# Kernel optimization log

Hardware: AMD Instinct MI355X
Metric: run time of the kernel (lower is better)

Reference implementation:

```python
import jax, jax.numpy as jnp
import numpy as np

GRANULARITY = 50
PERCENTILES = (0.01, 0.99)


def setup_inputs() -> dict:
    key = jax.random.key(0)
    H = W = 6144
    sp = jax.random.uniform(key, (H, W), dtype=jnp.float32)
    return {
        "signal_probabilities": sp,
        "rho_max": jnp.float32(H - 1),
        "rho_min": jnp.float32(0.0),
        "theta_min_horizontal": jnp.float32(0.01),
        "theta_max_horizontal": jnp.float32(0.05),
        "theta_min_vertical": jnp.float32(1.52),
        "theta_max_vertical": jnp.float32(1.56),
    }


def _linspace(a, b, n):
    t = jnp.arange(n, dtype=jnp.float32) / (n - 1)
    return a + (b - a) * t


def _fix_edge_effects(buf):
    buf = buf.at[0, :].set(buf[1, :])
    buf = buf.at[-1, :].set(buf[-2, :])
    buf = buf.at[:, 0].set(buf[:, 1])
    buf = buf.at[:, -1].set(buf[:, -2])
    return buf


def _fill_buffer(H, W, thetas, rhos, mode):
    # vectorized over all granularity lines at once (no python loop over lines)
    if mode == "horizontal":
        y = jnp.arange(H)
        # x[g, H]: x = -y*tan(theta) + rho/cos(theta)
        x = -y[None, :] * jnp.tan(thetas)[:, None] + (rhos / jnp.cos(thetas))[:, None]
        x = jnp.clip(jnp.round(x).astype(jnp.int32), 0, W - 1)
        yb = jnp.broadcast_to(y[None, :], x.shape)
        buf = jnp.zeros((H, W), jnp.int32).at[yb, x].add(1)
        buf = jnp.cumsum(buf, axis=1)
    else:
        x = jnp.arange(W)
        # y[g, W]: y = -x/tan(theta) + rho/sin(theta)
        y = -x[None, :] / jnp.tan(thetas)[:, None] + (rhos / jnp.sin(thetas))[:, None]
        y = jnp.clip(jnp.round(y).astype(jnp.int32), 0, H - 1)
        xb = jnp.broadcast_to(x[None, :], y.shape)
        buf = jnp.zeros((H, W), jnp.int32).at[y, xb].add(1)
        buf = jnp.cumsum(buf, axis=0)
    return _fix_edge_effects(buf)


def _get_bounds(nsp, thetas, rhos, mode):
    g = GRANULARITY
    H, W = nsp.shape
    buf = _fill_buffer(H, W, thetas, rhos, mode)
    # segment-sum replaces the dense one_hot * probs reduction (same math)
    values = jax.ops.segment_sum(nsp.reshape(-1), buf.reshape(-1), num_segments=g)
    c = jnp.cumsum(values) / jnp.sum(values)
    lower = jnp.argmax(c >= PERCENTILES[0])  # first index with cumsum >= p0
    upper = (g - 1) - jnp.argmax((c <= PERCENTILES[1])[::-1]) + 2  # last index with cumsum <= p1, +2
    return lower, upper


def _take_neg(a, i):
    # a[-i] with python-style negative indexing (i == 0 -> a[0])
    g = a.shape[0]
    return jnp.take(a, (g - i) % g)


def _intersect(r1, t1, r2, t2):
    det = jnp.cos(t1) * jnp.sin(t2) - jnp.cos(t2) * jnp.sin(t1)
    x = (r1 * jnp.sin(t2) - r2 * jnp.sin(t1)) / det
    y = (r2 * jnp.cos(t1) - r1 * jnp.cos(t2)) / det
    return jnp.stack((x, y))


def reference(signal_probabilities, rho_max, rho_min, theta_min_horizontal,
              theta_max_horizontal, theta_min_vertical, theta_max_vertical):
    g = GRANULARITY
    nsp = signal_probabilities - signal_probabilities.min()
    nsp = nsp / nsp.sum()
    rhos = _linspace(rho_max, rho_min, g)
    th = _linspace(theta_min_horizontal, theta_max_horizontal, g)
    tv = _linspace(theta_min_vertical, theta_max_vertical, g)
    lh, uh = _get_bounds(nsp, th, rhos, "horizontal")
    lv, uv = _get_bounds(nsp, tv, rhos, "vertical")
    r_min_h, r_max_h = _take_neg(rhos, lh), _take_neg(rhos, uh)
    t_min_h, t_max_h = _take_neg(th, lh), _take_neg(th, uh)
    r_min_v, r_max_v = _take_neg(rhos, lv), _take_neg(rhos, uv)
    t_min_v, t_max_v = _take_neg(tv, lv), _take_neg(tv, uv)
    # [top-left, top-right, bottom-right, bottom-left] -> shape (4, 2)
    return jnp.stack([
        _intersect(r_min_h, t_min_h, r_min_v, t_min_v),
        _intersect(r_max_h, t_max_h, r_min_v, t_min_v),
        _intersect(r_max_h, t_max_h, r_max_v, t_max_v),
        _intersect(r_min_h, t_min_h, r_max_v, t_max_v),
    ], axis=0)
```

## Files before the change

### kernel.cpp

```cpp
#include <hip/hip_runtime.h>
#include <math.h>

#define HH 6144
#define WW 6144
constexpr int G = 50;
constexpr int NCOPY = 64;
constexpr int NG = NCOPY * G;
constexpr int BIG = 0x0FFFFFFF;
constexpr int MINBASE = 4 * NG;
constexpr int CTR = MINBASE + NCOPY;
constexpr int MASTER = CTR + NCOPY;
constexpr int C0 = MASTER + 2;

constexpr int TPB  = 384;
constexpr int PXT  = 16;
constexpr int NBLK = HH;

__device__ inline void ldsAddF(float* p, float v)      { __hip_atomic_fetch_add(p, v, __ATOMIC_RELAXED, __HIP_MEMORY_SCOPE_WORKGROUP); }
__device__ inline void ldsAddU(unsigned* p, unsigned v){ __hip_atomic_fetch_add(p, v, __ATOMIC_RELAXED, __HIP_MEMORY_SCOPE_WORKGROUP); }
__device__ inline void ldsMinU(unsigned* p, unsigned v){ __hip_atomic_fetch_min(p, v, __ATOMIC_RELAXED, __HIP_MEMORY_SCOPE_WORKGROUP); }
__device__ inline void glbAddF(float* p, float v)      { __hip_atomic_fetch_add(p, v, __ATOMIC_RELAXED, __HIP_MEMORY_SCOPE_AGENT); }
__device__ inline void glbAddU(unsigned* p, unsigned v){ __hip_atomic_fetch_add(p, v, __ATOMIC_RELAXED, __HIP_MEMORY_SCOPE_AGENT); }
__device__ inline void glbMinU(unsigned* p, unsigned v){ __hip_atomic_fetch_min(p, v, __ATOMIC_RELAXED, __HIP_MEMORY_SCOPE_AGENT); }
__device__ inline unsigned glbAddCtr(unsigned* p)      { return __hip_atomic_fetch_add(p, 1u, __ATOMIC_RELAXED, __HIP_MEMORY_SCOPE_AGENT); }
__device__ inline float atomLoadF(const float* p)      { return __hip_atomic_load(p, __ATOMIC_RELAXED, __HIP_MEMORY_SCOPE_AGENT); }
__device__ inline unsigned atomLoadU(const unsigned* p){ return __hip_atomic_load(p, __ATOMIC_RELAXED, __HIP_MEMORY_SCOPE_AGENT); }

__global__ void crop_init(unsigned int* __restrict__ ws,
                          const float* __restrict__ p_rmax,
                          const float* __restrict__ p_rmin,
                          const float* __restrict__ p_thmin,
                          const float* __restrict__ p_thmax,
                          const float* __restrict__ p_tvmin,
                          const float* __restrict__ p_tvmax) {
  int i = blockIdx.x * 256 + threadIdx.x;
  if (i < MINBASE) ws[i] = 0u;
  else if (i < MINBASE + NCOPY) ws[i] = 0x7F800000u;
  else if (i < C0) ws[i] = 0u;

  if (blockIdx.x == 0 && threadIdx.x < G) {
    int t = threadIdx.x;
    double u    = (double)t / (double)(G - 1);
    double rmax = (double)p_rmax[0], rmin = (double)p_rmin[0];
    double rho  = rmax + (rmin - rmax) * u;
    double th   = (double)p_thmin[0] + ((double)p_thmax[0] - (double)p_thmin[0]) * u;
    double tv   = (double)p_tvmin[0] + ((double)p_tvmax[0] - (double)p_tvmin[0]) * u;
    double cth = cos(th), sth = sin(th);
    double ctv = cos(tv), stv = sin(tv);
    double* dT   = (double*)(ws + C0);
    double* dRC  = (double*)(ws + C0 + 100);
    float*  fva  = (float*)(ws + C0 + 200);
    float*  fvb  = (float*)(ws + C0 + 250);
    double* dRho = (double*)(ws + C0 + 300);
    double* dSth = (double*)(ws + C0 + 400);
    double* dCth = (double*)(ws + C0 + 500);
    double* dStv = (double*)(ws + C0 + 600);
    double* dCtv = (double*)(ws + C0 + 700);
    dT[t]  = tan(th);
    dRC[t] = rho / cth;
    fva[t] = (float)(rho / stv);
    fvb[t] = (float)(ctv / stv);
    dRho[t] = rho; dSth[t] = sth; dCth[t] = cth; dStv[t] = stv; dCtv[t] = ctv;
  }
}

__launch_bounds__(TPB)
__global__ void crop_main(const float* __restrict__ sp,
                          float* __restrict__ wsf,
                          float* __restrict__ out) {
  __shared__ int pxh[G], pxv[G];
  __shared__ float hsum[G + 1], vsum[G + 1];
  __shared__ unsigned int hcnt[G + 1], vcnt[G + 1];
  __shared__ unsigned int blockMinBits;
  __shared__ double valD[100];

  const int t  = threadIdx.x;
  const int y  = blockIdx.x;
  const int yp = min(max(y, 1), HH - 2);
  const float fyp = (float)yp;
  const int x0 = t * PXT;

  const float4* p4 = (const float4*)(sp + (size_t)y * WW + x0);
  float4 q0 = p4[0], q1 = p4[1], q2 = p4[2], q3 = p4[3];

  for (int i = t; i < G + 1; i += TPB) { hsum[i] = 0.f; vsum[i] = 0.f; hcnt[i] = 0u; vcnt[i] = 0u; }
  if (t == TPB - 1) blockMinBits = 0x7F800000u;

  const unsigned int* wsu = (const unsigned int*)wsf;
  if (t < G) {
    const double* dT  = (const double*)(wsu + C0);
    const double* dRC = (const double*)(wsu + C0 + 100);
    const float*  fva = (const float*)(wsu + C0 + 200);
    const float*  fvb = (const float*)(wsu + C0 + 250);

    double xg = rint(fma(-(double)yp, dT[t], dRC[t]));
    xg = fmin(fmax(xg, 0.0), (double)(WW - 1));
    int xi = (int)xg;
    pxh[t] = (xi <= 1) ? 0 : (xi >= WW - 1 ? BIG : xi);

    float va = fva[t], vb = fvb[t];
    int lo = 1, hi = WW - 1;
    while (lo < hi) {
      int m = (lo + hi) >> 1;
      float yv = rintf(fmaf(-(float)m, vb, va));
      yv = fminf(fmaxf(yv, 0.f), (float)(HH - 1));
      if (yv <= fyp) hi = m; else lo = m + 1;
    }
    pxv[t] = (lo >= WW - 1) ? BIG : (lo == 1 ? 0 : lo);
  }
  __syncthreads();

  float px[PXT] = { q0.x,q0.y,q0.z,q0.w, q1.x,q1.y,q1.z,q1.w,
                    q2.x,q2.y,q2.z,q2.w, q3.x,q3.y,q3.z,q3.w };

  int lo = 0, hi = G;
  while (lo < hi) { int m = (lo + hi) >> 1; if (pxh[m] <= x0) hi = m; else lo = m + 1; }
  const int lbh = lo;
  const int nbh = (lbh > 0) ? pxh[lbh - 1] : BIG;
  const int kh  = min(nbh - x0, PXT);

  lo = 0; hi = G;
  while (lo < hi) { int m = (lo + hi) >> 1; if (pxv[m] <= x0) hi = m; else lo = m + 1; }
  const int lbv = lo;
  const int nbv = (lbv > 0) ? pxv[lbv - 1] : BIG;
  const int kv  = min(nbv - x0, PXT);

  const int sh = G - lbh, sv = G - lbv;

  float S = 0.f, Ah = 0.f, Av = 0.f, mn = 3.4e38f;
#pragma unroll
  for (int k = 0; k < PXT; ++k) {
    float v = px[k];
    mn = fminf(mn, v);
    S += v;
    if (k + 1 == kh) Ah = S;
    if (k + 1 == kv) Av = S;
  }

  ldsAddF(&hsum[sh], Ah); ldsAddU(&hcnt[sh], (unsigned)kh);
  if (kh < PXT) { ldsAddF(&hsum[sh + 1], S - Ah); ldsAddU(&hcnt[sh + 1], (unsigned)(PXT - kh)); }
  ldsAddF(&vsum[sv], Av); ldsAddU(&vcnt[sv], (unsigned)kv);
  if (kv < PXT) { ldsAddF(&vsum[sv + 1], S - Av); ldsAddU(&vcnt[sv + 1], (unsigned)(PXT - kv)); }

  for (int off = 32; off; off >>= 1) mn = fminf(mn, __shfl_down(mn, off));
  if ((t & 63) == 0) ldsMinU(&blockMinBits, __float_as_uint(mn));

  __syncthreads();

  if (t >= 64) return;

  const int copy = y & (NCOPY - 1);
  unsigned int* wsw = (unsigned int*)wsf;
  if (t < G) {
    glbAddF(&wsf[copy * G + t], hsum[t]);
    glbAddU(&wsw[2 * NG + copy * G + t], hcnt[t]);
    glbAddF(&wsf[NG + copy * G + t], vsum[t]);
    glbAddU(&wsw[3 * NG + copy * G + t], vcnt[t]);
  }
  if (t == 0) glbMinU(&wsw[MINBASE + copy], blockMinBits);

  asm volatile("s_waitcnt vmcnt(0)" ::: "memory");

  int last = 0;
  if (t == 0) {
    unsigned p1 = glbAddCtr(&wsw[CTR + copy]);
    if (p1 == (unsigned)(NBLK / NCOPY - 1)) {
      unsigned p2 = glbAddCtr(&wsw[MASTER]);
      last = (p2 == (unsigned)(NCOPY - 1));
    }
  }
  last = __shfl(last, 0);
  if (!last) return;

  float vmn = __uint_as_float(atomLoadU(&wsu[MINBASE + t]));
  for (int off = 32; off; off >>= 1) vmn = fminf(vmn, __shfl_down(vmn, off));
  const double mv = (double)__shfl(vmn, 0);

  for (int p = t; p < 100; p += 64) {
    const int fam = p >= G;
    const int g = fam ? p - G : p;
    const int sumBase = fam ? NG : 0;
    const int cntBase = (2 + fam) * NG;
    double s = 0.0; unsigned c = 0;
#pragma unroll 8
    for (int cp = 0; cp < NCOPY; ++cp) {
      s += (double)atomLoadF(&wsf[sumBase + cp * G + g]);
      c += atomLoadU(&wsu[cntBase + cp * G + g]);
    }
    valD[p] = s - mv * (double)c;
  }
  asm volatile("s_waitcnt lgkmcnt(0)" ::: "memory");
  __builtin_amdgcn_sched_barrier(0);

  if (t == 0) {
    auto bounds = [&](int base, int& lowerI, int& upperI) {
      double tot = 0;
      for (int s = 0; s < G; ++s) tot += valD[base + s];
      double c = 0; bool found = false; int lastI = -1; lowerI = 0;
      for (int s = 0; s < G; ++s) {
        c += valD[base + s];
        double cc = c / tot;
        if (!found && cc >= 0.01) { lowerI = s; found = true; }
        if (cc <= 0.99) lastI = s;
      }
      upperI = (lastI < 0) ? (G + 1) : (lastI + 2);
    };
    int lh, uh, lv, uv;
    bounds(0, lh, uh);
    bounds(G, lv, uv);

    const double* dRho = (const double*)(wsu + C0 + 300);
    const double* dSth = (const double*)(wsu + C0 + 400);
    const double* dCth = (const double*)(wsu + C0 + 500);
    const double* dStv = (const double*)(wsu + C0 + 600);
    const double* dCtv = (const double*)(wsu + C0 + 700);

    auto tn = [&](int i) { return ((G - i) % G + G) % G; };
    int ihmin = tn(lh), ihmax = tn(uh), ivmin = tn(lv), ivmax = tn(uv);

    auto inter = [&](int ih, int iv, float* o) {
      double r1 = dRho[ih], s1 = dSth[ih], c1 = dCth[ih];
      double r2 = dRho[iv], s2 = dStv[iv], c2 = dCtv[iv];
      double det = c1 * s2 - c2 * s1;
      o[0] = (float)((r1 * s2 - r2 * s1) / det);
      o[1] = (float)((r2 * c1 - r1 * c2) / det);
    };
    inter(ihmin, ivmin, out + 0);
    inter(ihmax, ivmin, out + 2);
    inter(ihmax, ivmax, out + 4);
    inter(ihmin, ivmax, out + 6);
  }
}

extern "C" void kernel_launch(void* const* d_in, const int* in_sizes, int n_in,
                              void* d_out, int out_size, void* d_ws, size_t ws_size,
                              hipStream_t stream) {
  const float* sp    = (const float*)d_in[0];
  const float* rmax  = (const float*)d_in[1];
  const float* rmin  = (const float*)d_in[2];
  const float* thmin = (const float*)d_in[3];
  const float* thmax = (const float*)d_in[4];
  const float* tvmin = (const float*)d_in[5];
  const float* tvmax = (const float*)d_in[6];
  float* wsf  = (float*)d_ws;
  float* outp = (float*)d_out;

  crop_init<<<(C0 + 255) / 256, 256, 0, stream>>>((unsigned int*)d_ws,
                                                  rmax, rmin, thmin, thmax, tvmin, tvmax);
  crop_main<<<NBLK, TPB, 0, stream>>>(sp, wsf, outp);
}
```

Measured before the change: 251.6 us.

## Precompute per-row line boundaries in separate kernel and drop block barriers

```diff
diff --git a/kernel.cpp b/kernel.cpp
--- a/kernel.cpp
+++ b/kernel.cpp
@@ -11,14 +11,16 @@
 constexpr int CTR = MINBASE + NCOPY;
 constexpr int MASTER = CTR + NCOPY;
 constexpr int C0 = MASTER + 2;
+constexpr int PXHB = C0 + 800;
+constexpr int PXVB = PXHB + HH * G;
 
 constexpr int TPB  = 384;
 constexpr int PXT  = 16;
 constexpr int NBLK = HH;
+constexpr unsigned WPC = (HH / NCOPY) * (TPB / 64);
 
 __device__ inline void ldsAddF(float* p, float v)      { __hip_atomic_fetch_add(p, v, __ATOMIC_RELAXED, __HIP_MEMORY_SCOPE_WORKGROUP); }
 __device__ inline void ldsAddU(unsigned* p, unsigned v){ __hip_atomic_fetch_add(p, v, __ATOMIC_RELAXED, __HIP_MEMORY_SCOPE_WORKGROUP); }
-__device__ inline void ldsMinU(unsigned* p, unsigned v){ __hip_atomic_fetch_min(p, v, __ATOMIC_RELAXED, __HIP_MEMORY_SCOPE_WORKGROUP); }
 __device__ inline void glbAddF(float* p, float v)      { __hip_atomic_fetch_add(p, v, __ATOMIC_RELAXED, __HIP_MEMORY_SCOPE_AGENT); }
 __device__ inline void glbAddU(unsigned* p, unsigned v){ __hip_atomic_fetch_add(p, v, __ATOMIC_RELAXED, __HIP_MEMORY_SCOPE_AGENT); }
 __device__ inline void glbMinU(unsigned* p, unsigned v){ __hip_atomic_fetch_min(p, v, __ATOMIC_RELAXED, __HIP_MEMORY_SCOPE_AGENT); }
@@ -64,69 +66,84 @@
   }
 }
 
+__global__ void crop_bounds(unsigned int* __restrict__ ws) {
+  const int idx = blockIdx.x * 256 + threadIdx.x;
+  if (idx >= HH * G) return;
+  const int row = idx / G, g = idx - row * G;
+  const int yq = min(max(row, 1), HH - 2);
+  const float fyq = (float)yq;
+
+  const double* dT  = (const double*)(ws + C0);
+  const double* dRC = (const double*)(ws + C0 + 100);
+  const float*  fva = (const float*)(ws + C0 + 200);
+  const float*  fvb = (const float*)(ws + C0 + 250);
+
+  double xg = rint(fma(-(double)yq, dT[g], dRC[g]));
+  xg = fmin(fmax(xg, 0.0), (double)(WW - 1));
+  int xi = (int)xg;
+  ((int*)ws)[PXHB + idx] = (xi <= 1) ? 0 : (xi >= WW - 1 ? BIG : xi);
+
+  float va = fva[g], vb = fvb[g];
+  int lo = 1, hi = WW - 1;
+  while (lo < hi) {
+    int m = (lo + hi) >> 1;
+    float yv = rintf(fmaf(-(float)m, vb, va));
+    yv = fminf(fmaxf(yv, 0.f), (float)(HH - 1));
+    if (yv <= fyq) hi = m; else lo = m + 1;
+  }
+  ((int*)ws)[PXVB + idx] = (lo >= WW - 1) ? BIG : (lo == 1 ? 0 : lo);
+}
+
 __launch_bounds__(TPB)
 __global__ void crop_main(const float* __restrict__ sp,
                           float* __restrict__ wsf,
                           float* __restrict__ out) {
-  __shared__ int pxh[G], pxv[G];
-  __shared__ float hsum[G + 1], vsum[G + 1];
-  __shared__ unsigned int hcnt[G + 1], vcnt[G + 1];
-  __shared__ unsigned int blockMinBits;
+  __shared__ float    sH[TPB / 64][G + 2], sV[TPB / 64][G + 2];
+  __shared__ unsigned cH[TPB / 64][G + 2], cV[TPB / 64][G + 2];
   __shared__ double valD[100];
 
-  const int t  = threadIdx.x;
-  const int y  = blockIdx.x;
-  const int yp = min(max(y, 1), HH - 2);
-  const float fyp = (float)yp;
+  const int t = threadIdx.x, y = blockIdx.x;
+  const int w = t >> 6, lane = t & 63;
   const int x0 = t * PXT;
 
   const float4* p4 = (const float4*)(sp + (size_t)y * WW + x0);
   float4 q0 = p4[0], q1 = p4[1], q2 = p4[2], q3 = p4[3];
 
-  for (int i = t; i < G + 1; i += TPB) { hsum[i] = 0.f; vsum[i] = 0.f; hcnt[i] = 0u; vcnt[i] = 0u; }
-  if (t == TPB - 1) blockMinBits = 0x7F800000u;
-
-  const unsigned int* wsu = (const unsigned int*)wsf;
-  if (t < G) {
-    const double* dT  = (const double*)(wsu + C0);
-    const double* dRC = (const double*)(wsu + C0 + 100);
-    const float*  fva = (const float*)(wsu + C0 + 200);
-    const float*  fvb = (const float*)(wsu + C0 + 250);
-
-    double xg = rint(fma(-(double)yp, dT[t], dRC[t]));
-    xg = fmin(fmax(xg, 0.0), (double)(WW - 1));
-    int xi = (int)xg;
-    pxh[t] = (xi <= 1) ? 0 : (xi >= WW - 1 ? BIG : xi);
-
-    float va = fva[t], vb = fvb[t];
-    int lo = 1, hi = WW - 1;
-    while (lo < hi) {
-      int m = (lo + hi) >> 1;
-      float yv = rintf(fmaf(-(float)m, vb, va));
-      yv = fminf(fmaxf(yv, 0.f), (float)(HH - 1));
-      if (yv <= fyp) hi = m; else lo = m + 1;
-    }
-    pxv[t] = (lo >= WW - 1) ? BIG : (lo == 1 ? 0 : lo);
-  }
-  __syncthreads();
+  const int* ph = (const int*)wsf + PXHB + y * G;
+  const int* pv = (const int*)wsf + PXVB + y * G;
+  int bh = (lane < G) ? ph[lane] : BIG;
+  int bv = (lane < G) ? pv[lane] : BIG;
+
+  if (lane < G + 2) { sH[w][lane] = 0.f; cH[w][lane] = 0u; sV[w][lane] = 0.f; cV[w][lane] = 0u; }
+
+  int lo = 0, hi = G;
+#pragma unroll
+  for (int it = 0; it < 6; ++it) {
+    int m = (lo + hi) >> 1;
+    int pm = __shfl(bh, m);
+    if (lo < hi) { if (pm <= x0) hi = m; else lo = m + 1; }
+  }
+  const int lbh = lo;
+  int nbp = __shfl(bh, lbh > 0 ? lbh - 1 : 0);
+  const int nbh = (lbh > 0) ? nbp : BIG;
+  const int kh  = min(nbh - x0, PXT);
+
+  lo = 0; hi = G;
+#pragma unroll
+  for (int it = 0; it < 6; ++it) {
+    int m = (lo + hi) >> 1;
+    int pm = __shfl(bv, m);
+    if (lo < hi) { if (pm <= x0) hi = m; else lo = m + 1; }
+  }
+  const int lbv = lo;
+  nbp = __shfl(bv, lbv > 0 ? lbv - 1 : 0);
+  const int nbv = (lbv > 0) ? nbp : BIG;
+  const int kv  = min(nbv - x0, PXT);
+
+  const int sh = G - lbh, sv = G - lbv;
 
   float px[PXT] = { q0.x,q0.y,q0.z,q0.w, q1.x,q1.y,q1.z,q1.w,
                     q2.x,q2.y,q2.z,q2.w, q3.x,q3.y,q3.z,q3.w };
-
-  int lo = 0, hi = G;
-  while (lo < hi) { int m = (lo + hi) >> 1; if (pxh[m] <= x0) hi = m; else lo = m + 1; }
-  const int lbh = lo;
-  const int nbh = (lbh > 0) ? pxh[lbh - 1] : BIG;
-  const int kh  = min(nbh - x0, PXT);
-
-  lo = 0; hi = G;
-  while (lo < hi) { int m = (lo + hi) >> 1; if (pxv[m] <= x0) hi = m; else lo = m + 1; }
-  const int lbv = lo;
-  const int nbv = (lbv > 0) ? pxv[lbv - 1] : BIG;
-  const int kv  = min(nbv - x0, PXT);
-
-  const int sh = G - lbh, sv = G - lbv;
-
   float S = 0.f, Ah = 0.f, Av = 0.f, mn = 3.4e38f;
 #pragma unroll
   for (int k = 0; k < PXT; ++k) {
@@ -137,34 +154,33 @@
     if (k + 1 == kv) Av = S;
   }
 
-  ldsAddF(&hsum[sh], Ah); ldsAddU(&hcnt[sh], (unsigned)kh);
-  if (kh < PXT) { ldsAddF(&hsum[sh + 1], S - Ah); ldsAddU(&hcnt[sh + 1], (unsigned)(PXT - kh)); }
-  ldsAddF(&vsum[sv], Av); ldsAddU(&vcnt[sv], (unsigned)kv);
-  if (kv < PXT) { ldsAddF(&vsum[sv + 1], S - Av); ldsAddU(&vcnt[sv + 1], (unsigned)(PXT - kv)); }
+  ldsAddF(&sH[w][sh], Ah); ldsAddU(&cH[w][sh], (unsigned)kh);
+  if (kh < PXT) { ldsAddF(&sH[w][sh + 1], S - Ah); ldsAddU(&cH[w][sh + 1], (unsigned)(PXT - kh)); }
+  ldsAddF(&sV[w][sv], Av); ldsAddU(&cV[w][sv], (unsigned)kv);
+  if (kv < PXT) { ldsAddF(&sV[w][sv + 1], S - Av); ldsAddU(&cV[w][sv + 1], (unsigned)(PXT - kv)); }
 
   for (int off = 32; off; off >>= 1) mn = fminf(mn, __shfl_down(mn, off));
-  if ((t & 63) == 0) ldsMinU(&blockMinBits, __float_as_uint(mn));
-
-  __syncthreads();
-
-  if (t >= 64) return;
+
+  asm volatile("s_waitcnt lgkmcnt(0)" ::: "memory");
+  __builtin_amdgcn_sched_barrier(0);
 
   const int copy = y & (NCOPY - 1);
   unsigned int* wsw = (unsigned int*)wsf;
-  if (t < G) {
-    glbAddF(&wsf[copy * G + t], hsum[t]);
-    glbAddU(&wsw[2 * NG + copy * G + t], hcnt[t]);
-    glbAddF(&wsf[NG + copy * G + t], vsum[t]);
-    glbAddU(&wsw[3 * NG + copy * G + t], vcnt[t]);
-  }
-  if (t == 0) glbMinU(&wsw[MINBASE + copy], blockMinBits);
+  const unsigned int* wsu = (const unsigned int*)wsf;
+  if (lane < G) {
+    float    hs = sH[w][lane], vs = sV[w][lane];
+    unsigned hc = cH[w][lane], vc = cV[w][lane];
+    if (hc) { glbAddF(&wsf[copy * G + lane], hs); glbAddU(&wsw[2 * NG + copy * G + lane], hc); }
+    if (vc) { glbAddF(&wsf[NG + copy * G + lane], vs); glbAddU(&wsw[3 * NG + copy * G + lane], vc); }
+  }
+  if (lane == 0) glbMinU(&wsw[MINBASE + copy], __float_as_uint(mn));
 
   asm volatile("s_waitcnt vmcnt(0)" ::: "memory");
 
   int last = 0;
-  if (t == 0) {
+  if (lane == 0) {
     unsigned p1 = glbAddCtr(&wsw[CTR + copy]);
-    if (p1 == (unsigned)(NBLK / NCOPY - 1)) {
+    if (p1 == WPC - 1u) {
       unsigned p2 = glbAddCtr(&wsw[MASTER]);
       last = (p2 == (unsigned)(NCOPY - 1));
     }
@@ -172,11 +188,11 @@
   last = __shfl(last, 0);
   if (!last) return;
 
-  float vmn = __uint_as_float(atomLoadU(&wsu[MINBASE + t]));
+  float vmn = __uint_as_float(atomLoadU(&wsu[MINBASE + lane]));
   for (int off = 32; off; off >>= 1) vmn = fminf(vmn, __shfl_down(vmn, off));
   const double mv = (double)__shfl(vmn, 0);
 
-  for (int p = t; p < 100; p += 64) {
+  for (int p = lane; p < 100; p += 64) {
     const int fam = p >= G;
     const int g = fam ? p - G : p;
     const int sumBase = fam ? NG : 0;
@@ -192,7 +208,7 @@
   asm volatile("s_waitcnt lgkmcnt(0)" ::: "memory");
   __builtin_amdgcn_sched_barrier(0);
 
-  if (t == 0) {
+  if (lane == 0) {
     auto bounds = [&](int base, int& lowerI, int& upperI) {
       double tot = 0;
       for (int s = 0; s < G; ++s) tot += valD[base + s];
@@ -247,5 +263,6 @@
 
   crop_init<<<(C0 + 255) / 256, 256, 0, stream>>>((unsigned int*)d_ws,
                                                   rmax, rmin, thmin, thmax, tvmin, tvmax);
+  crop_bounds<<<(HH * G + 255) / 256, 256, 0, stream>>>((unsigned int*)d_ws);
   crop_main<<<NBLK, TPB, 0, stream>>>(sp, wsf, outp);
 }
```

Measured after the change: 381.1 us. 51.5% more time.
